# Kernel optimization log

Measured on AMD Instinct MI355X. Metric: run time of the kernel, lower is better.

Reference implementation:

```python
import jax, jax.numpy as jnp
import numpy as np

B, S, H, NH, HD = 2, 2048, 1024, 16, 64
THETA = 10000.0


def setup_inputs() -> dict:
    key = jax.random.key(0)
    k1, k2, k3, k4, k5 = jax.random.split(key, 5)
    hidden_states = jax.random.normal(k1, (B, S, H), dtype=jnp.float32)
    # RoPE tables, interleaved-pair layout: [c0,c0,c1,c1,...] along head_dim
    inv_freq = 1.0 / (THETA ** (jnp.arange(0, HD, 2, dtype=jnp.float32) / HD))
    t = jnp.arange(S, dtype=jnp.float32)
    freqs = jnp.outer(t, inv_freq)                      # [S, HD//2]
    freqs_cos = jnp.repeat(jnp.cos(freqs), 2, axis=-1)  # [S, HD]
    freqs_sin = jnp.repeat(jnp.sin(freqs), 2, axis=-1)  # [S, HD]
    position_ids = jnp.arange(S, dtype=jnp.int32)
    w = 0.02
    Wq = jax.random.normal(k2, (H, H), dtype=jnp.float32) * w
    Wk = jax.random.normal(k3, (H, H), dtype=jnp.float32) * w
    Wv = jax.random.normal(k4, (H, H), dtype=jnp.float32) * w
    Wo = jax.random.normal(k5, (H, H), dtype=jnp.float32) * w
    return {"hidden_states": hidden_states, "freqs_cos": freqs_cos,
            "freqs_sin": freqs_sin, "position_ids": position_ids,
            "Wq": Wq, "Wk": Wk, "Wv": Wv, "Wo": Wo}


def _rotate_half_interleaved(x):
    # stack([-x[..., 1::2], x[..., ::2]], -1).reshape_as(x)
    xe = x.reshape(x.shape[:-1] + (HD // 2, 2))
    return jnp.stack([-xe[..., 1], xe[..., 0]], axis=-1).reshape(x.shape)


def reference(hidden_states, freqs_cos, freqs_sin, position_ids, Wq, Wk, Wv, Wo):
    b, s, _ = hidden_states.shape
    # QKV projections (torch Linear: y = x @ W.T), split into heads [b, nh, s, hd]
    q = jnp.einsum('bsh,oh->bso', hidden_states, Wq).reshape(b, s, NH, HD).transpose(0, 2, 1, 3)
    k = jnp.einsum('bsh,oh->bso', hidden_states, Wk).reshape(b, s, NH, HD).transpose(0, 2, 1, 3)
    v = jnp.einsum('bsh,oh->bso', hidden_states, Wv).reshape(b, s, NH, HD).transpose(0, 2, 1, 3)
    cos = freqs_cos[position_ids][None, None]  # [1, 1, s, hd]
    sin = freqs_sin[position_ids][None, None]
    rq = _rotate_half_interleaved(q)
    # NOTE: faithful to source bug — rotate_half_k is built from q, not k
    q = q * cos + rq * sin
    k = k * cos + rq * sin
    # causal SDPA, scale = 1/sqrt(head_dim)
    scores = jnp.einsum('bhqd,bhkd->bhqk', q, k) / jnp.sqrt(jnp.float32(HD))
    causal = jnp.tril(jnp.ones((s, s), dtype=bool))
    scores = jnp.where(causal, scores, jnp.float32(-1e30))
    attn = jax.nn.softmax(scores, axis=-1)
    out = jnp.einsum('bhqk,bhkd->bhqd', attn, v)
    out = out.transpose(0, 2, 1, 3).reshape(b, s, H)
    return jnp.einsum('bsh,oh->bso', out, Wo)
```

## Files before the change

kernel.cpp:

```cpp
#include <hip/hip_runtime.h>
#include <stdint.h>

#define BB 2
#define SS 2048
#define HH 1024
#define NHH 16
#define HDD 64

typedef short bf16s;
typedef __attribute__((ext_vector_type(8))) short short8;
typedef __attribute__((ext_vector_type(4))) short short4v;
typedef __attribute__((ext_vector_type(2))) short short2v;
typedef __attribute__((ext_vector_type(4))) float f32x4;
typedef _Float16 half4v __attribute__((ext_vector_type(4)));
typedef _Float16 half8v __attribute__((ext_vector_type(8)));
typedef __fp16 fp16x2 __attribute__((ext_vector_type(2)));

__device__ inline short f2bf(float f) {
  union { float f; uint32_t u; } v; v.f = f;
  uint32_t r = (v.u + 0x7fffu + ((v.u >> 16) & 1u)) >> 16;
  return (short)r;
}
__device__ inline float bf2f(short h) {
  union { uint32_t u; float f; } v; v.u = ((uint32_t)(uint16_t)h) << 16;
  return v.f;
}

__device__ __forceinline__ float exp2_raw(float x) {
  float r;
  asm("v_exp_f32 %0, %1\n\ts_nop 0" : "=v"(r) : "v"(x));
  return r;
}

__device__ inline void gld_lds16(const void* g, void* l) {
  __builtin_amdgcn_global_load_lds((const __attribute__((address_space(1))) void*)g,
                                   (__attribute__((address_space(3))) void*)l, 16, 0, 0);
}

__device__ inline void stv(short* C, size_t i, float v) { C[i] = f2bf(v); }
__device__ inline void stv(float* C, size_t i, float v) { C[i] = v; }

__device__ inline f32x4 mfma_k32(short8 a, short8 b, f32x4 c) {
  return __builtin_amdgcn_mfma_f32_16x16x32_bf16(a, b, c, 0, 0, 0);
}
__device__ inline f32x4 mfma_k32(half8v a, half8v b, f32x4 c) {
  return __builtin_amdgcn_mfma_f32_16x16x32_f16(a, b, c, 0, 0, 0);
}
template <typename ET> struct ftr;
template <> struct ftr<short>     { using v8 = short8; };
template <> struct ftr<_Float16>  { using v8 = half8v; };

__global__ __launch_bounds__(256) void convert_all(
    const float* __restrict__ x, const float* __restrict__ Wq,
    const float* __restrict__ Wk, const float* __restrict__ Wv,
    const float* __restrict__ Wo, bf16s* __restrict__ xb,
    bf16s* __restrict__ wqkv, _Float16* __restrict__ wof) {
  const long M1 = 1024L * 1024L;
  long e = (long)(blockIdx.x * blockDim.x + threadIdx.x) * 4;
  if (e < 7 * M1) {
    const float* src; bf16s* dst;
    if (e < 4 * M1)      { src = x  + e;            dst = xb   + e; }
    else if (e < 5 * M1) { src = Wq + (e - 4 * M1); dst = wqkv + (e - 4 * M1); }
    else if (e < 6 * M1) { src = Wk + (e - 5 * M1); dst = wqkv + (e - 4 * M1); }
    else                 { src = Wv + (e - 6 * M1); dst = wqkv + (e - 4 * M1); }
    float4 v = *(const float4*)src;
    short4v o;
    o.x = f2bf(v.x); o.y = f2bf(v.y); o.z = f2bf(v.z); o.w = f2bf(v.w);
    *(short4v*)dst = o;
  } else {
    float4 v = *(const float4*)(Wo + (e - 7 * M1));
    half4v o;
    o.x = (_Float16)v.x; o.y = (_Float16)v.y;
    o.z = (_Float16)v.z; o.w = (_Float16)v.w;
    *(half4v*)(wof + (e - 7 * M1)) = o;
  }
}

template <typename ET, typename OT, int MT>
__global__ __launch_bounds__(256) void gemm_bt(
    const ET* __restrict__ A, const ET* __restrict__ Bm,
    OT* __restrict__ C, int K, int ldc) {
  using V8 = typename ftr<ET>::v8;
  __shared__ __align__(16) ET As[MT * 32 * 64];
  __shared__ __align__(16) ET Bs[128 * 64];
  const int tid = threadIdx.x;
  const int lane = tid & 63, w = tid >> 6;
  const int quad = lane >> 4, mcol = lane & 15;
  const int bm = blockIdx.y * (MT * 32), bn = blockIdx.x * 128;
  const int wm = (w >> 1) * (MT * 16), wn = (w & 1) * 64;
  f32x4 acc[MT][4] = {};
  const int nkt = K >> 6;
  for (int kt = 0; kt < nkt; ++kt) {
    __syncthreads();
#pragma unroll
    for (int i = 0; i < MT; ++i) {
      int seg = (i * 4 + w) * 512;
      int flat = seg + lane * 8;
      int row = flat >> 6;
      int cpos = (flat >> 3) & 7;
      int cs = cpos ^ (row & 7);
      gld_lds16(A + (size_t)(bm + row) * K + kt * 64 + cs * 8, &As[seg]);
    }
#pragma unroll
    for (int i = 0; i < 4; ++i) {
      int seg = (i * 4 + w) * 512;
      int flat = seg + lane * 8;
      int row = flat >> 6;
      int cpos = (flat >> 3) & 7;
      int cs = cpos ^ (row & 7);
      gld_lds16(Bm + (size_t)(bn + row) * K + kt * 64 + cs * 8, &Bs[seg]);
    }
    __syncthreads();
#pragma unroll
    for (int ks = 0; ks < 2; ++ks) {
      V8 af[MT], bf[4];
#pragma unroll
      for (int mt = 0; mt < MT; ++mt) {
        int row = wm + mt * 16 + mcol;
        int cs = (ks * 4 + quad) ^ (row & 7);
        af[mt] = *(const V8*)&As[row * 64 + cs * 8];
      }
#pragma unroll
      for (int nt = 0; nt < 4; ++nt) {
        int row = wn + nt * 16 + mcol;
        int cs = (ks * 4 + quad) ^ (row & 7);
        bf[nt] = *(const V8*)&Bs[row * 64 + cs * 8];
      }
#pragma unroll
      for (int mt = 0; mt < MT; ++mt)
#pragma unroll
        for (int nt = 0; nt < 4; ++nt)
          acc[mt][nt] = mfma_k32(af[mt], bf[nt], acc[mt][nt]);
    }
  }
#pragma unroll
  for (int mt = 0; mt < MT; ++mt)
#pragma unroll
    for (int nt = 0; nt < 4; ++nt) {
      int r0 = bm + wm + mt * 16 + quad * 4;
      int c = bn + wn + nt * 16 + mcol;
#pragma unroll
      for (int r = 0; r < 4; ++r)
        stv(C, (size_t)(r0 + r) * ldc + c, acc[mt][nt][r]);
    }
}

__global__ __launch_bounds__(256) void postproc(
    const bf16s* __restrict__ qkv, const float* __restrict__ fcos,
    const float* __restrict__ fsin, const int* __restrict__ pos,
    bf16s* __restrict__ Q, bf16s* __restrict__ Kc, _Float16* __restrict__ Vt) {
  const float LOG2E = 1.4426950408889634f;
  const int st = blockIdx.x, bh = blockIdx.y;
  const int b = bh >> 4, h = bh & 15;
  const int tid = threadIdx.x;
  const int m0 = b * 2048 + st * 64;
  {
    const int row = tid >> 2, pc = tid & 3;
    const int s = st * 64 + row;
    const int p = pos[s];
    const bf16s* qp = qkv + (size_t)(m0 + row) * 3072 + h * 64 + pc * 16;
    short8 qv[2] = { *(const short8*)qp, *(const short8*)(qp + 8) };
    short8 kv[2] = { *(const short8*)(qp + 1024), *(const short8*)(qp + 1032) };
    const float* cp = fcos + (size_t)p * 64 + pc * 16;
    const float* sp = fsin + (size_t)p * 64 + pc * 16;
    short8 qo[2], ko[2];
#pragma unroll
    for (int hf = 0; hf < 2; ++hf)
#pragma unroll
      for (int j = 0; j < 4; ++j) {
        float c = cp[hf * 8 + 2 * j], sn = sp[hf * 8 + 2 * j];
        float q0 = bf2f(qv[hf][2 * j]), q1 = bf2f(qv[hf][2 * j + 1]);
        float k0 = bf2f(kv[hf][2 * j]), k1 = bf2f(kv[hf][2 * j + 1]);
        qo[hf][2 * j]     = f2bf((q0 * c - q1 * sn) * 0.125f);
        qo[hf][2 * j + 1] = f2bf((q1 * c + q0 * sn) * 0.125f);
        ko[hf][2 * j]     = f2bf((k0 * c - q1 * sn) * LOG2E);
        ko[hf][2 * j + 1] = f2bf((k1 * c + q0 * sn) * LOG2E);
      }
    size_t o = ((size_t)bh * 2048 + s) * 64 + pc * 16;
    *(short8*)&Q[o] = qo[0];  *(short8*)&Q[o + 8] = qo[1];
    *(short8*)&Kc[o] = ko[0]; *(short8*)&Kc[o + 8] = ko[1];
  }
  __shared__ __align__(16) _Float16 T[64 * 72];
#pragma unroll
  for (int p2 = 0; p2 < 2; ++p2) {
    int sl = p2 * 32 + (tid >> 3);
    int ch = tid & 7;
    short8 v = *(const short8*)&qkv[(size_t)(m0 + sl) * 3072 + 2048 + h * 64 + ch * 8];
#pragma unroll
    for (int j = 0; j < 8; ++j) T[(ch * 8 + j) * 72 + sl] = (_Float16)bf2f(v[j]);
  }
  __syncthreads();
#pragma unroll
  for (int p2 = 0; p2 < 2; ++p2) {
    int dl = p2 * 32 + (tid >> 3);
    int ch = tid & 7;
    half8v v = *(const half8v*)&T[dl * 72 + ch * 8];
    *(half8v*)&Vt[((size_t)bh * 64 + dl) * 2048 + st * 64 + ch * 8] = v;
  }
}

template <bool DOB>
__device__ __forceinline__ void step2(
    const bf16s* __restrict__ Ks, const _Float16* __restrict__ Vp,
    const short8* bqA, const short8* bqB,
    f32x4* OA, f32x4* OB, float& lA, float& lB,
    bool diagA, bool diagB, int w, int quad, int col) {
  f32x4 sA[4], sB[4];
#pragma unroll
  for (int t = 0; t < 4; ++t) {
    f32x4 a = {}, bb = {};
#pragma unroll
    for (int ks = 0; ks < 2; ++ks) {
      int krow = t * 16 + col;
      int cs = (ks * 4 + quad) ^ (krow & 7);
      short8 af = *(const short8*)&Ks[krow * 64 + cs * 8];
      a = __builtin_amdgcn_mfma_f32_16x16x32_bf16(af, bqA[ks], a, 0, 0, 0);
      if (DOB) bb = __builtin_amdgcn_mfma_f32_16x16x32_bf16(af, bqB[ks], bb, 0, 0, 0);
    }
    sA[t] = a;
    if (DOB) sB[t] = bb;
  }
  if (diagA) {
#pragma unroll
    for (int t = 0; t < 4; ++t)
#pragma unroll
      for (int r = 0; r < 4; ++r)
        if (t * 16 + quad * 4 + r > w * 16 + col) sA[t][r] = -1e30f;
  }
  if (DOB && diagB) {
#pragma unroll
    for (int t = 0; t < 4; ++t)
#pragma unroll
      for (int r = 0; r < 4; ++r)
        if (t * 16 + quad * 4 + r > w * 16 + col) sB[t][r] = -1e30f;
  }
  half4v paA[4], paB[4];
#pragma unroll
  for (int t = 0; t < 4; ++t) {
    {
      float p0 = exp2_raw(sA[t][0]), p1 = exp2_raw(sA[t][1]);
      float p2 = exp2_raw(sA[t][2]), p3 = exp2_raw(sA[t][3]);
      lA += (p0 + p1) + (p2 + p3);
      union { fp16x2 h2[2]; half4v h4; } u;
      u.h2[0] = __builtin_amdgcn_cvt_pkrtz(p0, p1);
      u.h2[1] = __builtin_amdgcn_cvt_pkrtz(p2, p3);
      paA[t] = u.h4;
    }
    if (DOB) {
      float p0 = exp2_raw(sB[t][0]), p1 = exp2_raw(sB[t][1]);
      float p2 = exp2_raw(sB[t][2]), p3 = exp2_raw(sB[t][3]);
      lB += (p0 + p1) + (p2 + p3);
      union { fp16x2 h2[2]; half4v h4; } u;
      u.h2[0] = __builtin_amdgcn_cvt_pkrtz(p0, p1);
      u.h2[1] = __builtin_amdgcn_cvt_pkrtz(p2, p3);
      paB[t] = u.h4;
    }
  }
#pragma unroll
  for (int dt = 0; dt < 4; ++dt) {
    int vrow = dt * 16 + col;
    const _Float16* vp = &Vp[vrow * 72 + (quad ^ (vrow & 3)) * 16];
    union { half8v v8; half4v v4[2]; } a01, a23;
    a01.v8 = *(const half8v*)vp;
    a23.v8 = *(const half8v*)(vp + 8);
    half4v bv[4] = { a01.v4[0], a01.v4[1], a23.v4[0], a23.v4[1] };
#pragma unroll
    for (int t = 0; t < 4; ++t) {
      OA[dt] = __builtin_amdgcn_mfma_f32_16x16x16f16(paA[t], bv[t], OA[dt], 0, 0, 0);
      if (DOB) OB[dt] = __builtin_amdgcn_mfma_f32_16x16x16f16(paB[t], bv[t], OB[dt], 0, 0, 0);
    }
  }
}

__global__ __launch_bounds__(256) void attn(
    const bf16s* __restrict__ Q, const bf16s* __restrict__ Kb,
    const _Float16* __restrict__ Vt, _Float16* __restrict__ O) {
  __shared__ __align__(16) bf16s Ks[64 * 64];
  __shared__ __align__(16) _Float16 Vp[64 * 72];
  const int bh = blockIdx.y;
  const int tid = threadIdx.x, lane = tid & 63, w = tid >> 6;
  const int quad = lane >> 4, col = lane & 15;
  const size_t base = (size_t)bh * 2048 * 64;
  const _Float16* vbase = Vt + (size_t)bh * 64 * 2048;
  const int b = bh >> 4, h = bh & 15;
  const int x = blockIdx.x;
  const int qbA = 31 - x, qbB = x;

  short8 bqA[2], bqB[2];
  {
    const int qrA = qbA * 64 + w * 16 + col;
    const int qrB = qbB * 64 + w * 16 + col;
#pragma unroll
    for (int ks = 0; ks < 2; ++ks) {
      bqA[ks] = *(const short8*)&Q[base + (size_t)qrA * 64 + ks * 32 + quad * 8];
      bqB[ks] = *(const short8*)&Q[base + (size_t)qrB * 64 + ks * 32 + quad * 8];
    }
  }
  f32x4 OA[4] = {}, OB[4] = {};
  float lA = 0.f, lB = 0.f;

  const int vd = tid >> 2, vc = tid & 3;
  const int rot = vd & 3;
  for (int kt = 0; kt <= qbA; ++kt) {
    half8v vr0 = *(const half8v*)&vbase[(size_t)vd * 2048 + kt * 64 + vc * 16];
    half8v vr1 = *(const half8v*)&vbase[(size_t)vd * 2048 + kt * 64 + vc * 16 + 8];
    __syncthreads();
    {
      union { half8v v8; half4v v4[2]; } u0, u1;
      u0.v8 = vr0; u1.v8 = vr1;
      int rbase = vd * 72 + vc * 4;
      *(half4v*)&Vp[rbase + (0 ^ rot) * 16] = u0.v4[0];
      *(half4v*)&Vp[rbase + (1 ^ rot) * 16] = u0.v4[1];
      *(half4v*)&Vp[rbase + (2 ^ rot) * 16] = u1.v4[0];
      *(half4v*)&Vp[rbase + (3 ^ rot) * 16] = u1.v4[1];
    }
#pragma unroll
    for (int i = 0; i < 2; ++i) {
      int seg = (i * 4 + w) * 512;
      int flat = seg + lane * 8;
      int row = flat >> 6, cpos = (flat >> 3) & 7;
      int cs = cpos ^ (row & 7);
      gld_lds16(&Kb[base + (size_t)(kt * 64 + row) * 64 + cs * 8], &Ks[seg]);
    }
    __syncthreads();
    if (kt <= qbB)
      step2<true>(Ks, Vp, bqA, bqB, OA, OB, lA, lB,
                  false, kt == qbB, w, quad, col);
    else
      step2<false>(Ks, Vp, bqA, bqB, OA, OB, lA, lB,
                   kt == qbA, false, w, quad, col);
  }

  lA += __shfl_xor(lA, 16); lA += __shfl_xor(lA, 32);
  lB += __shfl_xor(lB, 16); lB += __shfl_xor(lB, 32);

#pragma unroll
  for (int which = 0; which < 2; ++which) {
    const int qb = which ? qbB : qbA;
    const f32x4* Oacc = which ? OB : OA;
    const float l = which ? lB : lA;
    float l4[4];
#pragma unroll
    for (int r = 0; r < 4; ++r) l4[r] = __shfl(l, quad * 4 + r);
#pragma unroll
    for (int dt = 0; dt < 4; ++dt)
#pragma unroll
      for (int r = 0; r < 4; ++r) {
        int srow = qb * 64 + w * 16 + quad * 4 + r;
        O[((size_t)b * 2048 + srow) * 1024 + h * 64 + dt * 16 + col] =
            (_Float16)(Oacc[dt][r] / l4[r]);
      }
  }
}

extern "C" void kernel_launch(void* const* d_in, const int* in_sizes, int n_in,
                              void* d_out, int out_size, void* d_ws, size_t ws_size,
                              hipStream_t stream) {
  (void)in_sizes; (void)n_in; (void)out_size; (void)ws_size;
  const float* x  = (const float*)d_in[0];
  const float* fc = (const float*)d_in[1];
  const float* fs = (const float*)d_in[2];
  const int* pos  = (const int*)d_in[3];
  const float* Wq = (const float*)d_in[4];
  const float* Wk = (const float*)d_in[5];
  const float* Wv = (const float*)d_in[6];
  const float* Wo = (const float*)d_in[7];
  float* out = (float*)d_out;
  char* ws = (char*)d_ws;
  const size_t MB = 1024 * 1024;
  bf16s* xb    = (bf16s*)(ws);
  bf16s* wqkv  = (bf16s*)(ws + 8 * MB);
  _Float16* wof = (_Float16*)(ws + 14 * MB);
  bf16s* qkv   = (bf16s*)(ws + 16 * MB);
  bf16s* Qb    = (bf16s*)(ws + 40 * MB);
  bf16s* Kb    = (bf16s*)(ws + 48 * MB);
  _Float16* Vt = (_Float16*)(ws + 56 * MB);
  _Float16* Ob = (_Float16*)(ws);

  convert_all<<<8192, 256, 0, stream>>>(x, Wq, Wk, Wv, Wo, xb, wqkv, wof);
  gemm_bt<short, short, 4><<<dim3(24, 32), 256, 0, stream>>>(xb, wqkv, qkv, 1024, 3072);
  postproc<<<dim3(32, 32), 256, 0, stream>>>(qkv, fc, fs, pos, Qb, Kb, Vt);
  attn<<<dim3(16, 32), 256, 0, stream>>>(Qb, Kb, Vt, Ob);
  gemm_bt<_Float16, float, 2><<<dim3(8, 64), 256, 0, stream>>>(Ob, wof, out, 1024, 1024);
}
```

Measured before the change: 191.3 us.

## Assign one query block per attention workgroup instead of paired blocks

The attention kernel previously gave each workgroup a pair of query blocks (31-x and x) so that causal work was balanced and each K/V tile load was shared by two query blocks. The change launches 32x32 workgroups, each handling one query block, which doubles the grid and removes the pairing. This adds parallelism and frees the registers used for the second accumulator, but it loses K/V tile reuse across paired blocks and brings back causal load imbalance across workgroups.

After: 205.9 us. 7.7% more time.

```diff
diff --git a/kernel.cpp b/kernel.cpp
--- a/kernel.cpp
+++ b/kernel.cpp
@@ -283,25 +283,21 @@
   const size_t base = (size_t)bh * 2048 * 64;
   const _Float16* vbase = Vt + (size_t)bh * 64 * 2048;
   const int b = bh >> 4, h = bh & 15;
-  const int x = blockIdx.x;
-  const int qbA = 31 - x, qbB = x;
-
-  short8 bqA[2], bqB[2];
+  const int qb = blockIdx.x;
+
+  short8 bq[2];
   {
-    const int qrA = qbA * 64 + w * 16 + col;
-    const int qrB = qbB * 64 + w * 16 + col;
-#pragma unroll
-    for (int ks = 0; ks < 2; ++ks) {
-      bqA[ks] = *(const short8*)&Q[base + (size_t)qrA * 64 + ks * 32 + quad * 8];
-      bqB[ks] = *(const short8*)&Q[base + (size_t)qrB * 64 + ks * 32 + quad * 8];
-    }
-  }
-  f32x4 OA[4] = {}, OB[4] = {};
-  float lA = 0.f, lB = 0.f;
+    const int qr = qb * 64 + w * 16 + col;
+#pragma unroll
+    for (int ks = 0; ks < 2; ++ks)
+      bq[ks] = *(const short8*)&Q[base + (size_t)qr * 64 + ks * 32 + quad * 8];
+  }
+  f32x4 OA[4] = {};
+  float lA = 0.f, lDummy = 0.f;
 
   const int vd = tid >> 2, vc = tid & 3;
   const int rot = vd & 3;
-  for (int kt = 0; kt <= qbA; ++kt) {
+  for (int kt = 0; kt <= qb; ++kt) {
     half8v vr0 = *(const half8v*)&vbase[(size_t)vd * 2048 + kt * 64 + vc * 16];
     half8v vr1 = *(const half8v*)&vbase[(size_t)vd * 2048 + kt * 64 + vc * 16 + 8];
     __syncthreads();
@@ -323,34 +319,23 @@
       gld_lds16(&Kb[base + (size_t)(kt * 64 + row) * 64 + cs * 8], &Ks[seg]);
     }
     __syncthreads();
-    if (kt <= qbB)
-      step2<true>(Ks, Vp, bqA, bqB, OA, OB, lA, lB,
-                  false, kt == qbB, w, quad, col);
-    else
-      step2<false>(Ks, Vp, bqA, bqB, OA, OB, lA, lB,
-                   kt == qbA, false, w, quad, col);
+    step2<false>(Ks, Vp, bq, bq, OA, OA, lA, lDummy,
+                 kt == qb, false, w, quad, col);
   }
 
   lA += __shfl_xor(lA, 16); lA += __shfl_xor(lA, 32);
-  lB += __shfl_xor(lB, 16); lB += __shfl_xor(lB, 32);
-
-#pragma unroll
-  for (int which = 0; which < 2; ++which) {
-    const int qb = which ? qbB : qbA;
-    const f32x4* Oacc = which ? OB : OA;
-    const float l = which ? lB : lA;
-    float l4[4];
-#pragma unroll
-    for (int r = 0; r < 4; ++r) l4[r] = __shfl(l, quad * 4 + r);
-#pragma unroll
-    for (int dt = 0; dt < 4; ++dt)
-#pragma unroll
-      for (int r = 0; r < 4; ++r) {
-        int srow = qb * 64 + w * 16 + quad * 4 + r;
-        O[((size_t)b * 2048 + srow) * 1024 + h * 64 + dt * 16 + col] =
-            (_Float16)(Oacc[dt][r] / l4[r]);
-      }
-  }
+
+  float l4[4];
+#pragma unroll
+  for (int r = 0; r < 4; ++r) l4[r] = __shfl(lA, quad * 4 + r);
+#pragma unroll
+  for (int dt = 0; dt < 4; ++dt)
+#pragma unroll
+    for (int r = 0; r < 4; ++r) {
+      int srow = qb * 64 + w * 16 + quad * 4 + r;
+      O[((size_t)b * 2048 + srow) * 1024 + h * 64 + dt * 16 + col] =
+          (_Float16)(OA[dt][r] / l4[r]);
+    }
 }
 
 extern "C" void kernel_launch(void* const* d_in, const int* in_sizes, int n_in,
@@ -380,6 +365,6 @@
   convert_all<<<8192, 256, 0, stream>>>(x, Wq, Wk, Wv, Wo, xb, wqkv, wof);
   gemm_bt<short, short, 4><<<dim3(24, 32), 256, 0, stream>>>(xb, wqkv, qkv, 1024, 3072);
   postproc<<<dim3(32, 32), 256, 0, stream>>>(qkv, fc, fs, pos, Qb, Kb, Vt);
-  attn<<<dim3(16, 32), 256, 0, stream>>>(Qb, Kb, Vt, Ob);
+  attn<<<dim3(32, 32), 256, 0, stream>>>(Qb, Kb, Vt, Ob);
   gemm_bt<_Float16, float, 2><<<dim3(8, 64), 256, 0, stream>>>(Ob, wof, out, 1024, 1024);
 }
```

## Double-buffer K and V tiles in attention kernel to overlap loads with compute

Applied to the files above, without the earlier changes.

Splits the shared-memory K and V tiles into two buffers and prefetches the next key tile (K via direct global-to-LDS loads, V via registers) while the current tile is processed. This cuts one barrier per iteration and is meant to hide global-memory latency behind the MFMA work. It doubles LDS use per block, which may reduce occupancy, and raises register pressure from holding the prefetched V values across the compute step.

Measured after the change: 197.4 us. 1.03x slower.

```diff
diff --git a/kernel.cpp b/kernel.cpp
--- a/kernel.cpp
+++ b/kernel.cpp
@@ -275,8 +275,8 @@
 __global__ __launch_bounds__(256) void attn(
     const bf16s* __restrict__ Q, const bf16s* __restrict__ Kb,
     const _Float16* __restrict__ Vt, _Float16* __restrict__ O) {
-  __shared__ __align__(16) bf16s Ks[64 * 64];
-  __shared__ __align__(16) _Float16 Vp[64 * 72];
+  __shared__ __align__(16) bf16s Ks[2][64 * 64];
+  __shared__ __align__(16) _Float16 Vp[2][64 * 72];
   const int bh = blockIdx.y;
   const int tid = threadIdx.x, lane = tid & 63, w = tid >> 6;
   const int quad = lane >> 4, col = lane & 15;
@@ -301,34 +301,61 @@
 
   const int vd = tid >> 2, vc = tid & 3;
   const int rot = vd & 3;
-  for (int kt = 0; kt <= qbA; ++kt) {
-    half8v vr0 = *(const half8v*)&vbase[(size_t)vd * 2048 + kt * 64 + vc * 16];
-    half8v vr1 = *(const half8v*)&vbase[(size_t)vd * 2048 + kt * 64 + vc * 16 + 8];
-    __syncthreads();
-    {
-      union { half8v v8; half4v v4[2]; } u0, u1;
-      u0.v8 = vr0; u1.v8 = vr1;
-      int rbase = vd * 72 + vc * 4;
-      *(half4v*)&Vp[rbase + (0 ^ rot) * 16] = u0.v4[0];
-      *(half4v*)&Vp[rbase + (1 ^ rot) * 16] = u0.v4[1];
-      *(half4v*)&Vp[rbase + (2 ^ rot) * 16] = u1.v4[0];
-      *(half4v*)&Vp[rbase + (3 ^ rot) * 16] = u1.v4[1];
-    }
+
+  {
+    half8v vr0 = *(const half8v*)&vbase[(size_t)vd * 2048 + vc * 16];
+    half8v vr1 = *(const half8v*)&vbase[(size_t)vd * 2048 + vc * 16 + 8];
 #pragma unroll
     for (int i = 0; i < 2; ++i) {
       int seg = (i * 4 + w) * 512;
       int flat = seg + lane * 8;
       int row = flat >> 6, cpos = (flat >> 3) & 7;
       int cs = cpos ^ (row & 7);
-      gld_lds16(&Kb[base + (size_t)(kt * 64 + row) * 64 + cs * 8], &Ks[seg]);
-    }
+      gld_lds16(&Kb[base + (size_t)row * 64 + cs * 8], &Ks[0][seg]);
+    }
+    union { half8v v8; half4v v4[2]; } u0, u1;
+    u0.v8 = vr0; u1.v8 = vr1;
+    int rbase = vd * 72 + vc * 4;
+    *(half4v*)&Vp[0][rbase + (0 ^ rot) * 16] = u0.v4[0];
+    *(half4v*)&Vp[0][rbase + (1 ^ rot) * 16] = u0.v4[1];
+    *(half4v*)&Vp[0][rbase + (2 ^ rot) * 16] = u1.v4[0];
+    *(half4v*)&Vp[0][rbase + (3 ^ rot) * 16] = u1.v4[1];
     __syncthreads();
+  }
+
+  for (int kt = 0; kt <= qbA; ++kt) {
+    const int cur = kt & 1, nxt = cur ^ 1;
+    const bool pf = (kt < qbA);
+    half8v vr0, vr1;
+    if (pf) {
+      vr0 = *(const half8v*)&vbase[(size_t)vd * 2048 + (kt + 1) * 64 + vc * 16];
+      vr1 = *(const half8v*)&vbase[(size_t)vd * 2048 + (kt + 1) * 64 + vc * 16 + 8];
+#pragma unroll
+      for (int i = 0; i < 2; ++i) {
+        int seg = (i * 4 + w) * 512;
+        int flat = seg + lane * 8;
+        int row = flat >> 6, cpos = (flat >> 3) & 7;
+        int cs = cpos ^ (row & 7);
+        gld_lds16(&Kb[base + (size_t)((kt + 1) * 64 + row) * 64 + cs * 8],
+                  &Ks[nxt][seg]);
+      }
+    }
     if (kt <= qbB)
-      step2<true>(Ks, Vp, bqA, bqB, OA, OB, lA, lB,
+      step2<true>(Ks[cur], Vp[cur], bqA, bqB, OA, OB, lA, lB,
                   false, kt == qbB, w, quad, col);
     else
-      step2<false>(Ks, Vp, bqA, bqB, OA, OB, lA, lB,
+      step2<false>(Ks[cur], Vp[cur], bqA, bqB, OA, OB, lA, lB,
                    kt == qbA, false, w, quad, col);
+    if (pf) {
+      union { half8v v8; half4v v4[2]; } u0, u1;
+      u0.v8 = vr0; u1.v8 = vr1;
+      int rbase = vd * 72 + vc * 4;
+      *(half4v*)&Vp[nxt][rbase + (0 ^ rot) * 16] = u0.v4[0];
+      *(half4v*)&Vp[nxt][rbase + (1 ^ rot) * 16] = u0.v4[1];
+      *(half4v*)&Vp[nxt][rbase + (2 ^ rot) * 16] = u1.v4[0];
+      *(half4v*)&Vp[nxt][rbase + (3 ^ rot) * 16] = u1.v4[1];
+    }
+    __syncthreads();
   }
 
   lA += __shfl_xor(lA, 16); lA += __shfl_xor(lA, 32);
```
